# Optimization experiments

Measured on AMD Instinct MI355X. Metric: run time of the kernel, lower is better.

Reference implementation:

```python
import jax, jax.numpy as jnp
import numpy as np

H = 128   # hidden_size
B = 8
TQ = 512  # num queries
TK = 512  # num keys


def setup_inputs() -> dict:
    key = jax.random.key(0)
    ks = jax.random.split(key, 8)
    s = 1.0 / np.sqrt(H)  # torch Linear default init bound
    return {
        "queries": jax.random.normal(ks[0], (B, TQ, H), dtype=jnp.float32),
        "keys": jax.random.normal(ks[1], (B, TK, H), dtype=jnp.float32),
        "Wa_w": jax.random.uniform(ks[2], (H, H), jnp.float32, -s, s),
        "Wa_b": jax.random.uniform(ks[3], (H,), jnp.float32, -s, s),
        "Ua_w": jax.random.uniform(ks[4], (H, H), jnp.float32, -s, s),
        "Ua_b": jax.random.uniform(ks[5], (H,), jnp.float32, -s, s),
        "Va_w": jax.random.uniform(ks[6], (H,), jnp.float32, -s, s),
        "Va_b": jax.random.uniform(ks[7], (), jnp.float32, -s, s),
    }


def reference(queries, keys, Wa_w, Wa_b, Ua_w, Ua_b, Va_w, Va_b):
    # Linear projections (torch Linear: y = x @ W.T + b)
    q = queries @ Wa_w.T + Wa_b                  # (B, Tq, H)
    k = keys @ Ua_w.T + Ua_b                     # (B, Tk, H)
    # Additive (Bahdanau) scores with broadcast intermediate (B, Tq, Tk, H)
    e = jnp.tanh(q[:, :, None, :] + k[:, None, :, :])
    scores = jnp.einsum('bqkh,h->bqk', e, Va_w) + Va_b  # (B, Tq, Tk)
    weights = jax.nn.softmax(scores, axis=-1)            # softmax over keys
    contexts = jnp.einsum('bqk,bkh->bqh', weights, keys) # (B, Tq, H)
    return contexts, weights
```

## Files before the change

### kernel.cpp

```cpp
#include <hip/hip_runtime.h>
#include <hip/hip_bf16.h>
#include <stdint.h>

#define HD 128
#define NB 8
#define TQN 512
#define TKN 512
#define QT 8
#define KTILE 64
#define KSTR 132
#define QSTR 132
#define KBSTR 136

typedef __attribute__((ext_vector_type(8))) short short8;
typedef __attribute__((ext_vector_type(4))) float f32x4;

static __device__ __forceinline__ float lo16(uint32_t w){
  union { uint32_t i; float f; } v; v.i = w << 16; return v.f;
}
static __device__ __forceinline__ float hi16(uint32_t w){
  union { uint32_t i; float f; } v; v.i = w & 0xffff0000u; return v.f;
}
static __device__ __forceinline__ float bf2f(unsigned short u){
  union { uint32_t i; float f; } v; v.i = ((uint32_t)u) << 16; return v.f;
}
static __device__ __forceinline__ uint32_t f2bf(float f){
  union { float f; uint32_t i; } v; v.f = f;
  uint32_t u = v.i;
  u += 0x7fffu + ((u >> 16) & 1u);
  return u >> 16;
}

static __device__ __forceinline__ float tanh_acc(float x){
  float e = __builtin_amdgcn_exp2f(x * 2.8853900817779268f);
  return fmaf(-2.0f, __builtin_amdgcn_rcpf(e + 1.0f), 1.0f);
}

static __device__ __forceinline__ float ld1(const void* p, size_t idx, bool f32){
  return f32 ? ((const float*)p)[idx] : bf2f(((const unsigned short*)p)[idx]);
}
static __device__ __forceinline__ short8 ld8bf(const void* p, size_t idx, bool f32){
  short8 r;
  if (f32){
    const float* s = (const float*)p + idx;
    #pragma unroll
    for (int i = 0; i < 8; i++) r[i] = (short)f2bf(s[i]);
  } else {
    r = *(const short8*)((const unsigned short*)p + idx);
  }
  return r;
}

static __device__ __forceinline__ void stage_keys(const void* keys, bool fK,
    unsigned short* keys_s, int b, int kt, int tid){
  if (fK){
    const float4* src = (const float4*)((const float*)keys + (size_t)(b*TKN + kt*KTILE)*HD);
    #pragma unroll
    for (int j = 0; j < 4; j++){
      const int f = tid + 512*j;
      float4 v = src[f];
      const int k = f >> 5;
      const int h = (f & 31) * 4;
      uint2 p;
      p.x = f2bf(v.x) | (f2bf(v.y) << 16);
      p.y = f2bf(v.z) | (f2bf(v.w) << 16);
      *(uint2*)(keys_s + k*KBSTR + h) = p;
    }
  } else {
    const uint4* src = (const uint4*)((const unsigned short*)keys + (size_t)(b*TKN + kt*KTILE)*HD);
    #pragma unroll
    for (int j = 0; j < 2; j++){
      const int f = tid + 512*j;
      uint4 v = src[f];
      const int k = f >> 4;
      const int h = (f & 15) * 8;
      *(uint4*)(keys_s + k*KBSTR + h) = v;
    }
  }
}

__global__ __launch_bounds__(512, 4) void fused_kernel(
    const void* __restrict__ queries, const void* __restrict__ keys,
    const void* __restrict__ Wa_w,   const void* __restrict__ Wa_b,
    const void* __restrict__ Ua_w,   const void* __restrict__ Ua_b,
    const void* __restrict__ Va_w,
    void* __restrict__ out)
{
  __shared__ float qp_s[QT*QSTR];
  __shared__ float va_s[HD];
  __shared__ __align__(16) unsigned short keys_s[KTILE*KBSTR];
  __shared__ __align__(16) float kp_s[KTILE*KSTR];
  __shared__ float sc_s[QT*TKN];
  __shared__ unsigned int flg_s[8];

  const int tid = threadIdx.x;

  if (tid < 8) flg_s[tid] = 0;
  __syncthreads();
  {
    const void* ptrs[7] = {queries, keys, Wa_w, Wa_b, Ua_w, Ua_b, Va_w};
    const int grp = tid >> 5;
    const int l   = tid & 31;
    if (grp < 7){
      const unsigned short* p = (const unsigned short*)ptrs[grp];
      unsigned short a = p[2*l];
      unsigned short c = p[64 + 2*l];
      if (((a >> 7) & 0xFF) > 0x90 || ((c >> 7) & 0xFF) > 0x90)
        atomicOr(&flg_s[grp], 1u);
    }
  }
  __syncthreads();
  const bool fQ  = flg_s[0] != 0;
  const bool fK  = flg_s[1] != 0;
  const bool fWw = flg_s[2] != 0;
  const bool fWb = flg_s[3] != 0;
  const bool fUw = flg_s[4] != 0;
  const bool fUb = flg_s[5] != 0;
  const bool fVw = flg_s[6] != 0;

  const int lane = tid & 63;
  const int wv   = tid >> 6;
  const int ln   = lane & 15;
  const int quad = lane >> 4;
  const int b     = blockIdx.x >> 6;
  const int qbase = (blockIdx.x & 63) * QT;

  if (tid < HD) va_s[tid] = ld1(Va_w, tid, fVw);

  {
    const int h0 = wv * 16;
    const size_t qrow = (size_t)(b*TQN + qbase + (ln & 7))*HD;
    f32x4 c = {0.f,0.f,0.f,0.f};
    #pragma unroll
    for (int ks = 0; ks < 4; ks++){
      short8 a = ld8bf(queries, qrow + ks*32 + quad*8, fQ);
      short8 w = ld8bf(Wa_w, (size_t)(h0 + ln)*HD + ks*32 + quad*8, fWw);
      c = __builtin_amdgcn_mfma_f32_16x16x32_bf16(a, w, c, 0,0,0);
    }
    const float wb = ld1(Wa_b, h0 + ln, fWb);
    #pragma unroll
    for (int r = 0; r < 4; r++){
      const int row = quad*4 + r;
      if (row < QT) qp_s[row*QSTR + h0 + ln] = tanh_acc(c[r] + wb);
    }
  }

  short8 ub[4];
  float ubias;
  {
    const int h0 = wv * 16;
    #pragma unroll
    for (int ks = 0; ks < 4; ks++)
      ub[ks] = ld8bf(Ua_w, (size_t)(h0 + ln)*HD + ks*32 + quad*8, fUw);
    ubias = ld1(Ua_b, h0 + ln, fUb);
  }

  stage_keys(keys, fK, keys_s, b, 0, tid);
  __syncthreads();

  const float4* q4p = (const float4*)(qp_s + wv*QSTR);
  const float4* v4p = (const float4*)va_s;

  for (int kt = 0; kt < 8; kt++){
    f32x4 kc[4];
    #pragma unroll
    for (int mt = 0; mt < 4; mt++) kc[mt] = (f32x4){0.f,0.f,0.f,0.f};
    #pragma unroll
    for (int ks = 0; ks < 4; ks++){
      short8 af[4];
      #pragma unroll
      for (int mt = 0; mt < 4; mt++)
        af[mt] = *(const short8*)(keys_s + (mt*16 + ln)*KBSTR + ks*32 + quad*8);
      #pragma unroll
      for (int mt = 0; mt < 4; mt++)
        kc[mt] = __builtin_amdgcn_mfma_f32_16x16x32_bf16(af[mt], ub[ks], kc[mt], 0,0,0);
    }
    __syncthreads();

    #pragma unroll
    for (int mt = 0; mt < 4; mt++)
      #pragma unroll
      for (int r = 0; r < 4; r++)
        kp_s[(mt*16 + quad*4 + r)*KSTR + wv*16 + ln] = tanh_acc(kc[mt][r] + ubias);
    if (kt < 7) stage_keys(keys, fK, keys_s, b, kt+1, tid);
    __syncthreads();

    float ac0 = 0.f, ac1 = 0.f, ac2 = 0.f, ac3 = 0.f;
    const float4* krow4 = (const float4*)(kp_s + lane*KSTR);
    #pragma unroll 8
    for (int hh = 0; hh < 32; hh++){
      const float4 tk = krow4[hh];
      const float4 tq = q4p[hh];
      const float4 vv = v4p[hh];
      float n0 = tq.x + tk.x, d0 = fmaf(tq.x, tk.x, 1.f);
      float n1 = tq.y + tk.y, d1 = fmaf(tq.y, tk.y, 1.f);
      float n2 = tq.z + tk.z, d2 = fmaf(tq.z, tk.z, 1.f);
      float n3 = tq.w + tk.w, d3 = fmaf(tq.w, tk.w, 1.f);
      ac0 = fmaf(vv.x * n0, __builtin_amdgcn_rcpf(d0), ac0);
      ac1 = fmaf(vv.y * n1, __builtin_amdgcn_rcpf(d1), ac1);
      ac2 = fmaf(vv.z * n2, __builtin_amdgcn_rcpf(d2), ac2);
      ac3 = fmaf(vv.w * n3, __builtin_amdgcn_rcpf(d3), ac3);
    }
    sc_s[wv*TKN + kt*KTILE + lane] = (ac0 + ac1) + (ac2 + ac3);
  }
  __syncthreads();

  {
    float vals[8];
    float m = -1e30f;
    #pragma unroll
    for (int j = 0; j < 8; j++){
      vals[j] = sc_s[wv*TKN + lane + 64*j];
      m = fmaxf(m, vals[j]);
    }
    #pragma unroll
    for (int o = 32; o > 0; o >>= 1) m = fmaxf(m, __shfl_xor(m, o));
    float sum = 0.f;
    #pragma unroll
    for (int j = 0; j < 8; j++){
      vals[j] = __builtin_amdgcn_exp2f((vals[j]-m)*1.4426950408889634f);
      sum += vals[j];
    }
    #pragma unroll
    for (int o = 32; o > 0; o >>= 1) sum += __shfl_xor(sum, o);
    const float inv = __builtin_amdgcn_rcpf(sum);
    const size_t wbase = (size_t)NB*TQN*HD + (size_t)(b*TQN + qbase + wv)*TKN;
    #pragma unroll
    for (int j = 0; j < 8; j++){
      const float w = vals[j]*inv;
      sc_s[wv*TKN + lane + 64*j] = w;
      if (fQ) ((float*)out)[wbase + lane + 64*j] = w;
      else    ((unsigned short*)out)[wbase + lane + 64*j] = (unsigned short)f2bf(w);
    }
  }
  __syncthreads();

  {
    const int h0 = ln * 8;
    float a[8];
    #pragma unroll
    for (int t = 0; t < 8; t++) a[t] = 0.f;
    for (int kt = 0; kt < 8; kt++){
      if (fK){
        const float4* src = (const float4*)((const float*)keys + (size_t)(b*TKN + kt*KTILE)*HD);
        #pragma unroll
        for (int j = 0; j < 4; j++){
          const int f = tid + 512*j;
          const int k = f >> 5;
          const int h = (f & 31) * 4;
          *(float4*)(kp_s + k*KSTR + h) = src[f];
        }
      } else {
        const uint4* src = (const uint4*)((const unsigned short*)keys + (size_t)(b*TKN + kt*KTILE)*HD);
        #pragma unroll
        for (int j = 0; j < 2; j++){
          const int f = tid + 512*j;
          const int k = f >> 4;
          const int h = (f & 15) * 8;
          uint4 v = src[f];
          float4 d0, d1;
          d0.x = lo16(v.x); d0.y = hi16(v.x); d0.z = lo16(v.y); d0.w = hi16(v.y);
          d1.x = lo16(v.z); d1.y = hi16(v.z); d1.z = lo16(v.w); d1.w = hi16(v.w);
          *(float4*)(kp_s + k*KSTR + h)     = d0;
          *(float4*)(kp_s + k*KSTR + h + 4) = d1;
        }
      }
      __syncthreads();
      const float* wr = sc_s + wv*TKN + kt*KTILE;
      #pragma unroll 4
      for (int i = 0; i < 16; i++){
        const int k = 4*i + quad;
        const float w = wr[k];
        const float4 k0 = *(const float4*)(kp_s + k*KSTR + h0);
        const float4 k1 = *(const float4*)(kp_s + k*KSTR + h0 + 4);
        a[0] = fmaf(w, k0.x, a[0]); a[1] = fmaf(w, k0.y, a[1]);
        a[2] = fmaf(w, k0.z, a[2]); a[3] = fmaf(w, k0.w, a[3]);
        a[4] = fmaf(w, k1.x, a[4]); a[5] = fmaf(w, k1.y, a[5]);
        a[6] = fmaf(w, k1.z, a[6]); a[7] = fmaf(w, k1.w, a[7]);
      }
      __syncthreads();
    }
    #pragma unroll
    for (int t = 0; t < 8; t++){
      a[t] += __shfl_xor(a[t], 16);
      a[t] += __shfl_xor(a[t], 32);
    }
    if (quad == 0){
      const size_t crow = (size_t)(b*TQN + qbase + wv)*HD + h0;
      if (fQ){
        float* oc = (float*)out;
        *(float4*)(oc + crow)     = (float4){a[0],a[1],a[2],a[3]};
        *(float4*)(oc + crow + 4) = (float4){a[4],a[5],a[6],a[7]};
      } else {
        uint4 o;
        o.x = f2bf(a[0]) | (f2bf(a[1]) << 16);
        o.y = f2bf(a[2]) | (f2bf(a[3]) << 16);
        o.z = f2bf(a[4]) | (f2bf(a[5]) << 16);
        o.w = f2bf(a[6]) | (f2bf(a[7]) << 16);
        *(uint4*)((unsigned short*)out + crow) = o;
      }
    }
  }
}

extern "C" void kernel_launch(void* const* d_in, const int* in_sizes, int n_in,
                              void* d_out, int out_size, void* d_ws, size_t ws_size,
                              hipStream_t stream) {
  (void)in_sizes; (void)n_in; (void)out_size; (void)d_ws; (void)ws_size;
  fused_kernel<<<512, 512, 0, stream>>>(d_in[0], d_in[1], d_in[2], d_in[3],
                                        d_in[4], d_in[5], d_in[6], d_out);
}
```

Measured before the change: 161.1 us.

## Register-cache query/Va slices in score loop and reuse key loads across two queries

The score loop is remapped so each lane holds a 16-element slice of the query and Va vectors in registers, with v*q precomputed. Each lane covers 8 keys, and partial sums are reduced with DPP adds instead of reading q and Va from LDS on every iteration. The context accumulation is also restructured: each wave handles two query rows over half the key tile, so each key LDS load feeds two rows. The two halves are combined through shared memory at the end. This trades more registers and an extra barrier plus partial-sum exchange for less LDS traffic.

```diff
diff --git a/kernel.cpp b/kernel.cpp
--- a/kernel.cpp
+++ b/kernel.cpp
@@ -34,6 +34,14 @@
 static __device__ __forceinline__ float tanh_acc(float x){
   float e = __builtin_amdgcn_exp2f(x * 2.8853900817779268f);
   return fmaf(-2.0f, __builtin_amdgcn_rcpf(e + 1.0f), 1.0f);
+}
+
+template<int CTRL>
+static __device__ __forceinline__ float dpp_add(float x){
+  union { float f; int i; } u; u.f = x;
+  int y = __builtin_amdgcn_update_dpp(0, u.i, CTRL, 0xf, 0xf, true);
+  union { int i; float f; } w; w.i = y;
+  return x + w.f;
 }
 
 static __device__ __forceinline__ float ld1(const void* p, size_t idx, bool f32){
@@ -158,8 +166,21 @@
   stage_keys(keys, fK, keys_s, b, 0, tid);
   __syncthreads();
 
-  const float4* q4p = (const float4*)(qp_s + wv*QSTR);
-  const float4* v4p = (const float4*)va_s;
+  const int s8 = lane >> 3;
+  const int o8 = lane & 7;
+  float tqr[16], var[16], vat[16];
+  {
+    const float* qsrc = qp_s + wv*QSTR + o8*16;
+    const float* vsrc = va_s + o8*16;
+    #pragma unroll
+    for (int c = 0; c < 4; c++){
+      float4 t = *(const float4*)(qsrc + c*4);
+      float4 v = *(const float4*)(vsrc + c*4);
+      tqr[c*4+0]=t.x; tqr[c*4+1]=t.y; tqr[c*4+2]=t.z; tqr[c*4+3]=t.w;
+      var[c*4+0]=v.x; var[c*4+1]=v.y; var[c*4+2]=v.z; var[c*4+3]=v.w;
+      vat[c*4+0]=v.x*t.x; vat[c*4+1]=v.y*t.y; vat[c*4+2]=v.z*t.z; vat[c*4+3]=v.w*t.w;
+    }
+  }
 
   for (int kt = 0; kt < 8; kt++){
     f32x4 kc[4];
@@ -185,23 +206,37 @@
     if (kt < 7) stage_keys(keys, fK, keys_s, b, kt+1, tid);
     __syncthreads();
 
-    float ac0 = 0.f, ac1 = 0.f, ac2 = 0.f, ac3 = 0.f;
-    const float4* krow4 = (const float4*)(kp_s + lane*KSTR);
-    #pragma unroll 8
-    for (int hh = 0; hh < 32; hh++){
-      const float4 tk = krow4[hh];
-      const float4 tq = q4p[hh];
-      const float4 vv = v4p[hh];
-      float n0 = tq.x + tk.x, d0 = fmaf(tq.x, tk.x, 1.f);
-      float n1 = tq.y + tk.y, d1 = fmaf(tq.y, tk.y, 1.f);
-      float n2 = tq.z + tk.z, d2 = fmaf(tq.z, tk.z, 1.f);
-      float n3 = tq.w + tk.w, d3 = fmaf(tq.w, tk.w, 1.f);
-      ac0 = fmaf(vv.x * n0, __builtin_amdgcn_rcpf(d0), ac0);
-      ac1 = fmaf(vv.y * n1, __builtin_amdgcn_rcpf(d1), ac1);
-      ac2 = fmaf(vv.z * n2, __builtin_amdgcn_rcpf(d2), ac2);
-      ac3 = fmaf(vv.w * n3, __builtin_amdgcn_rcpf(d3), ac3);
-    }
-    sc_s[wv*TKN + kt*KTILE + lane] = (ac0 + ac1) + (ac2 + ac3);
+    float acc[8];
+    #pragma unroll
+    for (int i = 0; i < 8; i++) acc[i] = 0.f;
+    #pragma unroll
+    for (int i = 0; i < 8; i++){
+      const float* tk = kp_s + (i*8 + s8)*KSTR + o8*16;
+      #pragma unroll
+      for (int c = 0; c < 4; c++){
+        const float4 kv = *(const float4*)(tk + c*4);
+        acc[i] = fmaf(fmaf(var[c*4+0], kv.x, vat[c*4+0]),
+                      __builtin_amdgcn_rcpf(fmaf(tqr[c*4+0], kv.x, 1.f)), acc[i]);
+        acc[i] = fmaf(fmaf(var[c*4+1], kv.y, vat[c*4+1]),
+                      __builtin_amdgcn_rcpf(fmaf(tqr[c*4+1], kv.y, 1.f)), acc[i]);
+        acc[i] = fmaf(fmaf(var[c*4+2], kv.z, vat[c*4+2]),
+                      __builtin_amdgcn_rcpf(fmaf(tqr[c*4+2], kv.z, 1.f)), acc[i]);
+        acc[i] = fmaf(fmaf(var[c*4+3], kv.w, vat[c*4+3]),
+                      __builtin_amdgcn_rcpf(fmaf(tqr[c*4+3], kv.w, 1.f)), acc[i]);
+      }
+    }
+    #pragma unroll
+    for (int i = 0; i < 8; i++){
+      float a = acc[i];
+      a = dpp_add<0xB1>(a);
+      a = dpp_add<0x4E>(a);
+      a = dpp_add<0x141>(a);
+      acc[i] = a;
+    }
+    float sc = acc[0];
+    #pragma unroll
+    for (int i = 1; i < 8; i++) sc = (o8 == i) ? acc[i] : sc;
+    sc_s[wv*TKN + kt*KTILE + o8*8 + s8] = sc;
   }
   __syncthreads();
 
@@ -236,10 +271,12 @@
   __syncthreads();
 
   {
+    const int p2 = wv & 3;
+    const int g2 = wv >> 2;
     const int h0 = ln * 8;
-    float a[8];
-    #pragma unroll
-    for (int t = 0; t < 8; t++) a[t] = 0.f;
+    float a0[8], a1[8];
+    #pragma unroll
+    for (int t = 0; t < 8; t++){ a0[t] = 0.f; a1[t] = 0.f; }
     for (int kt = 0; kt < 8; kt++){
       if (fK){
         const float4* src = (const float4*)((const float*)keys + (size_t)(b*TKN + kt*KTILE)*HD);
@@ -266,38 +303,65 @@
         }
       }
       __syncthreads();
-      const float* wr = sc_s + wv*TKN + kt*KTILE;
-      #pragma unroll 4
-      for (int i = 0; i < 16; i++){
-        const int k = 4*i + quad;
-        const float w = wr[k];
-        const float4 k0 = *(const float4*)(kp_s + k*KSTR + h0);
-        const float4 k1 = *(const float4*)(kp_s + k*KSTR + h0 + 4);
-        a[0] = fmaf(w, k0.x, a[0]); a[1] = fmaf(w, k0.y, a[1]);
-        a[2] = fmaf(w, k0.z, a[2]); a[3] = fmaf(w, k0.w, a[3]);
-        a[4] = fmaf(w, k1.x, a[4]); a[5] = fmaf(w, k1.y, a[5]);
-        a[6] = fmaf(w, k1.z, a[6]); a[7] = fmaf(w, k1.w, a[7]);
+      const float* w0r = sc_s + (2*p2)*TKN + kt*KTILE + g2*32;
+      const float* w1r = w0r + TKN;
+      #pragma unroll
+      for (int i = 0; i < 8; i++){
+        const int k = i*4 + quad;
+        const float w0 = w0r[k];
+        const float w1 = w1r[k];
+        const float* kr = kp_s + (g2*32 + k)*KSTR + h0;
+        const float4 k0 = *(const float4*)(kr);
+        const float4 k1 = *(const float4*)(kr + 4);
+        a0[0]=fmaf(w0,k0.x,a0[0]); a0[1]=fmaf(w0,k0.y,a0[1]);
+        a0[2]=fmaf(w0,k0.z,a0[2]); a0[3]=fmaf(w0,k0.w,a0[3]);
+        a0[4]=fmaf(w0,k1.x,a0[4]); a0[5]=fmaf(w0,k1.y,a0[5]);
+        a0[6]=fmaf(w0,k1.z,a0[6]); a0[7]=fmaf(w0,k1.w,a0[7]);
+        a1[0]=fmaf(w1,k0.x,a1[0]); a1[1]=fmaf(w1,k0.y,a1[1]);
+        a1[2]=fmaf(w1,k0.z,a1[2]); a1[3]=fmaf(w1,k0.w,a1[3]);
+        a1[4]=fmaf(w1,k1.x,a1[4]); a1[5]=fmaf(w1,k1.y,a1[5]);
+        a1[6]=fmaf(w1,k1.z,a1[6]); a1[7]=fmaf(w1,k1.w,a1[7]);
       }
       __syncthreads();
     }
     #pragma unroll
     for (int t = 0; t < 8; t++){
-      a[t] += __shfl_xor(a[t], 16);
-      a[t] += __shfl_xor(a[t], 32);
-    }
-    if (quad == 0){
-      const size_t crow = (size_t)(b*TQN + qbase + wv)*HD + h0;
+      a0[t] += __shfl_xor(a0[t], 16); a0[t] += __shfl_xor(a0[t], 32);
+      a1[t] += __shfl_xor(a1[t], 16); a1[t] += __shfl_xor(a1[t], 32);
+    }
+    float* part = qp_s;
+    if (g2 == 1 && quad == 0){
+      *(float4*)(part + (2*p2  )*HD + h0    ) = (float4){a0[0],a0[1],a0[2],a0[3]};
+      *(float4*)(part + (2*p2  )*HD + h0 + 4) = (float4){a0[4],a0[5],a0[6],a0[7]};
+      *(float4*)(part + (2*p2+1)*HD + h0    ) = (float4){a1[0],a1[1],a1[2],a1[3]};
+      *(float4*)(part + (2*p2+1)*HD + h0 + 4) = (float4){a1[4],a1[5],a1[6],a1[7]};
+    }
+    __syncthreads();
+    if (g2 == 0 && quad == 0){
+      const float4 p00 = *(const float4*)(part + (2*p2  )*HD + h0    );
+      const float4 p01 = *(const float4*)(part + (2*p2  )*HD + h0 + 4);
+      const float4 p10 = *(const float4*)(part + (2*p2+1)*HD + h0    );
+      const float4 p11 = *(const float4*)(part + (2*p2+1)*HD + h0 + 4);
+      const size_t crow0 = (size_t)(b*TQN + qbase + 2*p2    )*HD + h0;
+      const size_t crow1 = (size_t)(b*TQN + qbase + 2*p2 + 1)*HD + h0;
       if (fQ){
         float* oc = (float*)out;
-        *(float4*)(oc + crow)     = (float4){a[0],a[1],a[2],a[3]};
-        *(float4*)(oc + crow + 4) = (float4){a[4],a[5],a[6],a[7]};
+        *(float4*)(oc + crow0)     = (float4){a0[0]+p00.x, a0[1]+p00.y, a0[2]+p00.z, a0[3]+p00.w};
+        *(float4*)(oc + crow0 + 4) = (float4){a0[4]+p01.x, a0[5]+p01.y, a0[6]+p01.z, a0[7]+p01.w};
+        *(float4*)(oc + crow1)     = (float4){a1[0]+p10.x, a1[1]+p10.y, a1[2]+p10.z, a1[3]+p10.w};
+        *(float4*)(oc + crow1 + 4) = (float4){a1[4]+p11.x, a1[5]+p11.y, a1[6]+p11.z, a1[7]+p11.w};
       } else {
-        uint4 o;
-        o.x = f2bf(a[0]) | (f2bf(a[1]) << 16);
-        o.y = f2bf(a[2]) | (f2bf(a[3]) << 16);
-        o.z = f2bf(a[4]) | (f2bf(a[5]) << 16);
-        o.w = f2bf(a[6]) | (f2bf(a[7]) << 16);
-        *(uint4*)((unsigned short*)out + crow) = o;
+        uint4 o0, o1;
+        o0.x = f2bf(a0[0]+p00.x) | (f2bf(a0[1]+p00.y) << 16);
+        o0.y = f2bf(a0[2]+p00.z) | (f2bf(a0[3]+p00.w) << 16);
+        o0.z = f2bf(a0[4]+p01.x) | (f2bf(a0[5]+p01.y) << 16);
+        o0.w = f2bf(a0[6]+p01.z) | (f2bf(a0[7]+p01.w) << 16);
+        o1.x = f2bf(a1[0]+p10.x) | (f2bf(a1[1]+p10.y) << 16);
+        o1.y = f2bf(a1[2]+p10.z) | (f2bf(a1[3]+p10.w) << 16);
+        o1.z = f2bf(a1[4]+p11.x) | (f2bf(a1[5]+p11.y) << 16);
+        o1.w = f2bf(a1[6]+p11.z) | (f2bf(a1[7]+p11.w) << 16);
+        *(uint4*)((unsigned short*)out + crow0) = o0;
+        *(uint4*)((unsigned short*)out + crow1) = o1;
       }
     }
   }
```

Result: no change. 158.4 us (-1.7%).
